# Kernel optimization log

Hardware: AMD Instinct MI355X
Metric: run time of the kernel (lower is better)

## Reference

```python
import jax, jax.numpy as jnp
import numpy as np

EMBED_DIM = 256
H = 80
W = 80
N_HEADS = 8
N_POINTS = 4
B = 8


def sine_pe(C, h, w):
    # LoFTR-style PositionEncodingSine, returns [1, C, h, w]
    y_pos = jnp.cumsum(jnp.ones((h, w), jnp.float32), axis=0)[None]
    x_pos = jnp.cumsum(jnp.ones((h, w), jnp.float32), axis=1)[None]
    div = jnp.exp(jnp.arange(0, C // 2, 2, dtype=jnp.float32) * (-np.log(10000.0) / (C // 2)))[:, None, None]
    pe = jnp.zeros((C, h, w), jnp.float32)
    pe = pe.at[0::4].set(jnp.sin(x_pos * div))
    pe = pe.at[1::4].set(jnp.cos(x_pos * div))
    pe = pe.at[2::4].set(jnp.sin(y_pos * div))
    pe = pe.at[3::4].set(jnp.cos(y_pos * div))
    return pe[None]


def make_reference_points(h, w):
    # Faithful to the original (W-major flatten, (col, row) stacking)
    gr = np.linspace(0, 1, w)
    gc = np.linspace(0, 1, h)
    R, Cg = np.meshgrid(gr, gc, indexing='ij')  # (w, h)
    ref = np.stack((Cg, R), -1).reshape(-1, 2)  # [w*h, 2]
    return jnp.asarray(ref, jnp.float32)


def setup_inputs():
    key = jax.random.key(0)
    ks = jax.random.split(key, 8)
    C = EMBED_DIM
    s = 1.0 / np.sqrt(C)
    return {
        'query': jax.random.normal(ks[0], (B, C, H, W), jnp.float32),
        'value': jax.random.normal(ks[1], (B, C, H, W), jnp.float32),
        'W_value': jax.random.normal(ks[2], (C, C), jnp.float32) * s,
        'b_value': jnp.zeros((C,), jnp.float32),
        'W_off': jax.random.normal(ks[3], (C, N_HEADS * N_POINTS * 2), jnp.float32) * 0.01,
        'b_off': jax.random.normal(ks[4], (N_HEADS * N_POINTS * 2,), jnp.float32) * 0.5,
        'W_attn': jax.random.normal(ks[5], (C, N_HEADS * N_POINTS), jnp.float32) * s,
        'b_attn': jnp.zeros((N_HEADS * N_POINTS,), jnp.float32),
        'W_out': jax.random.normal(ks[6], (C, C), jnp.float32) * s,
        'b_out': jnp.zeros((C,), jnp.float32),
    }


def _deform_attn_core(q, v, ref, W_off, b_off, W_attn, b_attn):
    # q: [B, Nq, C] queries; v: [B, H*W, C] projected values; ref: [Nq, 2]
    Bq, Nq, C = q.shape
    hd = C // N_HEADS
    off = (q @ W_off + b_off).reshape(Bq, Nq, N_HEADS, N_POINTS, 2)
    aw = jax.nn.softmax((q @ W_attn + b_attn).reshape(Bq, Nq, N_HEADS, N_POINTS), axis=-1)
    norm = jnp.array([W, H], jnp.float32)  # offset normalizer (W, H), num_levels=1
    loc = ref[None, :, None, None, :] + off / norm  # [B, Nq, Hn, P, 2], normalized (x, y)
    loc = loc.transpose(0, 2, 1, 3, 4)  # [B, Hn, Nq, P, 2]
    # grid_sample(align_corners=False, padding_mode='zeros'): pixel = loc*size - 0.5
    x = loc[..., 0] * W - 0.5
    y = loc[..., 1] * H - 0.5
    x0f = jnp.floor(x); y0f = jnp.floor(y)
    wx = x - x0f; wy = y - y0f
    x0 = x0f.astype(jnp.int32); y0 = y0f.astype(jnp.int32)
    vh = v.reshape(Bq, H * W, N_HEADS, hd).transpose(0, 2, 1, 3)  # [B, Hn, HW, hd]

    def gather(ix, iy):
        valid = (ix >= 0) & (ix < W) & (iy >= 0) & (iy < H)
        idx = jnp.clip(iy, 0, H - 1) * W + jnp.clip(ix, 0, W - 1)  # [B, Hn, Nq, P]
        g = jnp.take_along_axis(vh, idx.reshape(Bq, N_HEADS, -1, 1), axis=2)
        return g.reshape(Bq, N_HEADS, Nq, N_POINTS, hd) * valid[..., None].astype(v.dtype)

    samp = (gather(x0, y0) * ((1 - wx) * (1 - wy))[..., None]
            + gather(x0 + 1, y0) * (wx * (1 - wy))[..., None]
            + gather(x0, y0 + 1) * ((1 - wx) * wy)[..., None]
            + gather(x0 + 1, y0 + 1) * (wx * wy)[..., None])  # [B, Hn, Nq, P, hd]
    out = jnp.einsum('bhqpd,bhqp->bqhd', samp, aw.transpose(0, 2, 1, 3))
    return out.reshape(Bq, Nq, C)


def reference(query, value, W_value, b_value, W_off, b_off, W_attn, b_attn, W_out, b_out):
    pe = sine_pe(EMBED_DIM, H, W)
    q = query + pe
    qf = q.reshape(B, EMBED_DIM, H * W).transpose(0, 2, 1)      # [B, Nq, C]
    vf = value.reshape(B, EMBED_DIM, H * W).transpose(0, 2, 1)  # [B, Nv, C]
    vproj = vf @ W_value + b_value
    ref = make_reference_points(H, W)
    attn = _deform_attn_core(qf, vproj, ref, W_off, b_off, W_attn, b_attn)
    attn = attn @ W_out + b_out
    attn = attn + qf  # mmcv MSDeformAttn residual (dropout identity at eval)
    out_img = attn.transpose(0, 2, 1).reshape(B, EMBED_DIM, H, W)
    # nn.Upsample(size=(H, W), bilinear) on an (H, W) map is identity (need_downsample=False)
    return (out_img + value, out_img)
```

## Files before the change

### kernel.cpp

```cpp
#include <hip/hip_runtime.h>
#include <hip/hip_bf16.h>
#include <stdint.h>

#define HH 80
#define WW 80
#define NQ 6400
#define CD 256
#define BB 8
#define OUT_HALF 13107200
#define PE_NEG 0.0719557841560639f

typedef __attribute__((ext_vector_type(4))) float f32x4;
typedef __bf16 bf16_t;
typedef __attribute__((ext_vector_type(8))) __bf16 bf16x8;

using gp1_t = const __attribute__((address_space(1))) void*;
using lp3_t = __attribute__((address_space(3))) void*;

__device__ __forceinline__ void gload_lds16(const void* g, void* l) {
    __builtin_amdgcn_global_load_lds((gp1_t)g, (lp3_t)l, 16, 0, 0);
}

__global__ __launch_bounds__(256) void wprep_kernel(const float* __restrict__ Wv,
                                                    const float* __restrict__ Woff,
                                                    const float* __restrict__ Wattn,
                                                    const float* __restrict__ Wout,
                                                    bf16_t* __restrict__ WvT,
                                                    bf16_t* __restrict__ WoaT,
                                                    bf16_t* __restrict__ WoT) {
    int idx = blockIdx.x * 256 + threadIdx.x;
    if (idx < 65536) {
        int cp = idx >> 8, c = idx & 255;
        WvT[idx] = (bf16_t)Wv[c * 256 + cp];
        WoT[idx] = (bf16_t)Wout[c * 256 + cp];
    }
    if (idx < 96 * 256) {
        int j = idx >> 8, c = idx & 255;
        WoaT[idx] = (bf16_t)(j < 64 ? Woff[c * 64 + j] : Wattn[c * 32 + (j - 64)]);
    }
}

__global__ __launch_bounds__(256, 3) void gemm_vproj(const float* __restrict__ V,
                                                     const bf16_t* __restrict__ Y,
                                                     const float* __restrict__ bias,
                                                     bf16_t* __restrict__ D) {
    __shared__ __align__(16) bf16_t lx[128 * 72];
    __shared__ __align__(16) bf16_t ly[128 * 64];
    int b = blockIdx.x & 7;
    int nloc = (blockIdx.x >> 3) * 128;
    int m0 = b * NQ + nloc;
    int c0 = blockIdx.y * 128;
    const float* src = V + (size_t)b * CD * NQ + nloc;
    int tid = threadIdx.x, wv = tid >> 6, ln = tid & 63;
    f32x4 acc[4][4] = {};
    int wr = (wv >> 1) * 64, wc = (wv & 1) * 64;
    int nl = tid & 31;
    for (int kt = 0; kt < 4; ++kt) {
#pragma unroll
        for (int q8 = 0; q8 < 4; ++q8) {
            int q = wv * 4 + q8;
            int row = q * 8 + (ln >> 3);
            int jj = (ln & 7) ^ (row & 7);
            gload_lds16((const char*)Y + ((size_t)(c0 + row)) * 512 + (size_t)kt * 128 + jj * 16,
                        (char*)ly + q * 1024);
        }
#pragma unroll
        for (int i = 0; i < 4; ++i) {
            int kp = (tid >> 5) + i * 8;
            int k = kp * 2;
            const float* s0 = src + (size_t)(kt * 64 + k) * NQ;
#pragma unroll
            for (int l = 0; l < 4; ++l) {
                int n = nl + 32 * l;
                float v0 = s0[n];
                float v1 = s0[NQ + n];
                union { bf16_t h[2]; uint32_t u; } pk;
                pk.h[0] = (bf16_t)v0; pk.h[1] = (bf16_t)v1;
                *(uint32_t*)((char*)lx + n * 144 + k * 2) = pk.u;
            }
        }
        __syncthreads();
#pragma unroll
        for (int ks = 0; ks < 2; ++ks) {
            bf16x8 xa[4], yb[4];
#pragma unroll
            for (int i = 0; i < 4; i++) {
                int m = wr + i * 16 + (ln & 15);
                xa[i] = *(const bf16x8*)((const char*)lx + m * 144 + ks * 64 + (ln >> 4) * 16);
                int n = wc + i * 16 + (ln & 15);
                int cn = (ks * 4 + (ln >> 4)) ^ (n & 7);
                yb[i] = *(const bf16x8*)((const char*)ly + n * 128 + cn * 16);
            }
#pragma unroll
            for (int i = 0; i < 4; i++)
#pragma unroll
                for (int j = 0; j < 4; j++)
                    acc[i][j] = __builtin_amdgcn_mfma_f32_16x16x32_bf16(xa[i], yb[j], acc[i][j], 0, 0, 0);
        }
        __syncthreads();
    }
#pragma unroll
    for (int i = 0; i < 4; i++)
#pragma unroll
        for (int j = 0; j < 4; j++) {
            int col = c0 + wc + j * 16 + (ln & 15);
            float bv = bias[col];
#pragma unroll
            for (int rg = 0; rg < 4; rg++) {
                int row = m0 + wr + i * 16 + (ln >> 4) * 4 + rg;
                D[(size_t)row * 256 + col] = (bf16_t)(acc[i][j][rg] + bv);
            }
        }
}

__global__ __launch_bounds__(256, 2) void oa_sample_out(
        const float* __restrict__ Q,
        const bf16_t* __restrict__ Woa,
        const float* __restrict__ boff,
        const float* __restrict__ battn,
        const bf16_t* __restrict__ vp,
        const bf16_t* __restrict__ WoT,
        const float* __restrict__ bout,
        const float* __restrict__ value,
        float* __restrict__ out) {
    __shared__ __align__(16) char smem[67072];
    char* sampL = smem;
    bf16_t* lx = (bf16_t*)(smem + 32768);
    bf16_t* ly = (bf16_t*)(smem + 41984);
    bf16_t* wx = (bf16_t*)(smem + 32768);
    float* tile = (float*)(smem + 32768);
    bf16_t* oaT = (bf16_t*)(smem + 54272);

    int bid = blockIdx.x;
    int b = bid & 7;
    int nloc = (bid >> 3) * 64;
    int tid = threadIdx.x, wv = tid >> 6, ln = tid & 63;
    const float* src = Q + (size_t)b * CD * NQ + nloc;
    int nl = tid & 31;

    {
        f32x4 acc[1][6] = {};
        for (int kt = 0; kt < 4; ++kt) {
#pragma unroll
            for (int q3 = 0; q3 < 3; ++q3) {
                int q = wv * 3 + q3;
                int row = q * 8 + (ln >> 3);
                int jj = (ln & 7) ^ (row & 7);
                gload_lds16((const char*)Woa + ((size_t)row) * 512 + (size_t)kt * 128 + jj * 16,
                            (char*)ly + q * 1024);
            }
#pragma unroll
            for (int i = 0; i < 4; ++i) {
                int kp = (tid >> 5) + i * 8;
                int k = kp * 2;
                int c = kt * 64 + k;
                float d = __expf((float)(2 * (c >> 2)) * -PE_NEG);
                const float* s0 = src + (size_t)c * NQ;
#pragma unroll
                for (int l = 0; l < 2; ++l) {
                    int n = nl + 32 * l;
                    int p = nloc + n;
                    int h = p / WW, w = p - h * WW;
                    float pos = (c & 2) ? (float)(h + 1) : (float)(w + 1);
                    float sv, cv;
                    __sincosf(pos * d, &sv, &cv);
                    float v0 = s0[n] + sv;
                    float v1 = s0[NQ + n] + cv;
                    union { bf16_t hh[2]; uint32_t u; } pk;
                    pk.hh[0] = (bf16_t)v0; pk.hh[1] = (bf16_t)v1;
                    *(uint32_t*)((char*)lx + n * 144 + k * 2) = pk.u;
                }
            }
            __syncthreads();
#pragma unroll
            for (int ks = 0; ks < 2; ++ks) {
                bf16x8 xa, yb[6];
                int m = wv * 16 + (ln & 15);
                xa = *(const bf16x8*)((const char*)lx + m * 144 + ks * 64 + (ln >> 4) * 16);
#pragma unroll
                for (int j = 0; j < 6; j++) {
                    int n = j * 16 + (ln & 15);
                    int cn = (ks * 4 + (ln >> 4)) ^ (n & 7);
                    yb[j] = *(const bf16x8*)((const char*)ly + n * 128 + cn * 16);
                }
#pragma unroll
                for (int j = 0; j < 6; j++)
                    acc[0][j] = __builtin_amdgcn_mfma_f32_16x16x32_bf16(xa, yb[j], acc[0][j], 0, 0, 0);
            }
            __syncthreads();
        }
#pragma unroll
        for (int j = 0; j < 6; j++) {
            int col = j * 16 + (ln & 15);
            float bv = col < 64 ? boff[col] : battn[col - 64];
#pragma unroll
            for (int rg = 0; rg < 4; rg++) {
                int rloc = wv * 16 + (ln >> 4) * 4 + rg;
                oaT[rloc * 100 + col] = (bf16_t)(acc[0][j][rg] + bv);
            }
        }
    }
    __syncthreads();

    {
        int h = (tid >> 1) & 7, sh = tid & 1;
        const bf16_t* vb = vp + (size_t)b * NQ * CD + h * 32 + sh * 16;
#pragma unroll
        for (int rnd = 0; rnd < 4; ++rnd) {
            int q = rnd * 16 + (tid >> 4);
            int n = nloc + q;
            const bf16_t* sq = oaT + q * 100;
            float l0 = (float)sq[64 + h * 4 + 0], l1 = (float)sq[64 + h * 4 + 1];
            float l2 = (float)sq[64 + h * 4 + 2], l3 = (float)sq[64 + h * 4 + 3];
            float mx = fmaxf(fmaxf(l0, l1), fmaxf(l2, l3));
            float e0 = __expf(l0 - mx), e1 = __expf(l1 - mx), e2 = __expf(l2 - mx), e3 = __expf(l3 - mx);
            float inv = 1.f / (e0 + e1 + e2 + e3);
            float aw[4] = {e0 * inv, e1 * inv, e2 * inv, e3 * inv};
            float xb = (float)(n % WW) * (80.f / 79.f) - 0.5f;
            float yb = (float)(n / WW) * (80.f / 79.f) - 0.5f;
            float wgt[16];
            int idx[16];
#pragma unroll
            for (int p = 0; p < 4; p++) {
                float x = xb + (float)sq[h * 8 + p * 2];
                float y = yb + (float)sq[h * 8 + p * 2 + 1];
                float x0f = floorf(x), y0f = floorf(y);
                float wx_ = x - x0f, wy_ = y - y0f;
                int ix = (int)x0f, iy = (int)y0f;
                bool vx0 = (unsigned)ix < (unsigned)WW, vx1 = (unsigned)(ix + 1) < (unsigned)WW;
                bool vy0 = (unsigned)iy < (unsigned)HH, vy1 = (unsigned)(iy + 1) < (unsigned)HH;
                int cx0 = min(max(ix, 0), WW - 1), cx1 = min(max(ix + 1, 0), WW - 1);
                int cy0 = min(max(iy, 0), HH - 1), cy1 = min(max(iy + 1, 0), HH - 1);
                float ap = aw[p];
                wgt[p * 4 + 0] = (vx0 && vy0) ? ap * (1.f - wx_) * (1.f - wy_) : 0.f;
                wgt[p * 4 + 1] = (vx1 && vy0) ? ap * wx_ * (1.f - wy_) : 0.f;
                wgt[p * 4 + 2] = (vx0 && vy1) ? ap * (1.f - wx_) * wy_ : 0.f;
                wgt[p * 4 + 3] = (vx1 && vy1) ? ap * wx_ * wy_ : 0.f;
                idx[p * 4 + 0] = cy0 * WW + cx0;
                idx[p * 4 + 1] = cy0 * WW + cx1;
                idx[p * 4 + 2] = cy1 * WW + cx0;
                idx[p * 4 + 3] = cy1 * WW + cx1;
            }
            float fac[16];
#pragma unroll
            for (int j = 0; j < 16; j++) fac[j] = 0.f;
#pragma unroll
            for (int pc = 0; pc < 16; ++pc) {
                const bf16x8* p8 = (const bf16x8*)(vb + (size_t)idx[pc] * CD);
                bf16x8 v0 = p8[0], v1 = p8[1];
                float w = wgt[pc];
#pragma unroll
                for (int j = 0; j < 8; j++) fac[j] += (float)v0[j] * w;
#pragma unroll
                for (int j = 0; j < 8; j++) fac[8 + j] += (float)v1[j] * w;
            }
            bf16x8 o0, o1;
#pragma unroll
            for (int j = 0; j < 8; j++) { o0[j] = (bf16_t)fac[j]; o1[j] = (bf16_t)fac[8 + j]; }
            int c0 = 4 * h + 2 * sh;
            *(bf16x8*)(sampL + q * 512 + ((c0 ^ (q & 7)) * 16)) = o0;
            *(bf16x8*)(sampL + q * 512 + (((c0 + 1) ^ (q & 7)) * 16)) = o1;
        }
    }
    __syncthreads();

    const float* qp = Q + (size_t)b * CD * NQ;
    const float* vvp = value + (size_t)b * CD * NQ;
    float* o0p = out + (size_t)b * CD * NQ;
    float* o1p = out + OUT_HALF + (size_t)b * CD * NQ;
    for (int p = 0; p < 2; ++p) {
        int cb = p * 128;
        f32x4 acc[4][2] = {};
        for (int kt = 0; kt < 4; ++kt) {
#pragma unroll
            for (int q8 = 0; q8 < 4; ++q8) {
                int q = wv * 4 + q8;
                int row = q * 8 + (ln >> 3);
                int jj = (ln & 7) ^ (row & 7);
                gload_lds16((const char*)WoT + ((size_t)(cb + row)) * 512 + (size_t)kt * 128 + jj * 16,
                            (char*)wx + q * 1024);
            }
            __syncthreads();
#pragma unroll
            for (int ks = 0; ks < 2; ++ks) {
                bf16x8 xa[4], yb[2];
#pragma unroll
                for (int i = 0; i < 4; i++) {
                    int m = (wv >> 1) * 64 + i * 16 + (ln & 15);
                    int ch = (ks * 4 + (ln >> 4)) ^ (m & 7);
                    xa[i] = *(const bf16x8*)((const char*)wx + m * 128 + ch * 16);
                }
#pragma unroll
                for (int j = 0; j < 2; j++) {
                    int nr = (wv & 1) * 32 + j * 16 + (ln & 15);
                    int cj = kt * 8 + ks * 4 + (ln >> 4);
                    yb[j] = *(const bf16x8*)(sampL + nr * 512 + ((cj ^ (nr & 7)) * 16));
                }
#pragma unroll
                for (int i = 0; i < 4; i++)
#pragma unroll
                    for (int j = 0; j < 2; j++)
                        acc[i][j] = __builtin_amdgcn_mfma_f32_16x16x32_bf16(xa[i], yb[j], acc[i][j], 0, 0, 0);
            }
            __syncthreads();
        }
#pragma unroll
        for (int hp = 0; hp < 2; ++hp) {
            if ((wv >> 1) == hp) {
#pragma unroll
                for (int i = 0; i < 4; i++)
#pragma unroll
                    for (int j = 0; j < 2; j++) {
                        int c = (wv & 1) * 32 + j * 16 + (ln & 15);
#pragma unroll
                        for (int rg = 0; rg < 4; rg++) {
                            int r = i * 16 + (ln >> 4) * 4 + rg;
                            tile[r * 68 + c] = acc[i][j][rg] + bout[cb + hp * 64 + r];
                        }
                    }
            }
            __syncthreads();
            int g4 = (tid & 15) * 4;
            int rowbase = tid >> 4;
#pragma unroll
            for (int jj = 0; jj < 4; ++jj) {
                int r = rowbase + jj * 16;
                int crow = cb + hp * 64 + r;
                size_t off = (size_t)crow * NQ + nloc + g4;
                f32x4 tv = *(const f32x4*)&tile[r * 68 + g4];
                f32x4 qv = *(const f32x4*)(qp + off);
                f32x4 vv = *(const f32x4*)(vvp + off);
                float d = __expf((float)(2 * (crow >> 2)) * -PE_NEG);
                bool useY = (crow & 2) != 0, odd = (crow & 1) != 0;
                f32x4 pv;
#pragma unroll
                for (int e = 0; e < 4; ++e) {
                    int n = nloc + g4 + e;
                    int hh = n / WW, ww = n - hh * WW;
                    float pos = useY ? (float)(hh + 1) : (float)(ww + 1);
                    float sv, cv;
                    __sincosf(pos * d, &sv, &cv);
                    pv[e] = odd ? cv : sv;
                }
                f32x4 o1v = tv + qv + pv;
                *(f32x4*)(o1p + off) = o1v;
                *(f32x4*)(o0p + off) = o1v + vv;
            }
            __syncthreads();
        }
    }
}

extern "C" void kernel_launch(void* const* d_in, const int* in_sizes, int n_in,
                              void* d_out, int out_size, void* d_ws, size_t ws_size,
                              hipStream_t stream) {
    const float* query   = (const float*)d_in[0];
    const float* value   = (const float*)d_in[1];
    const float* W_value = (const float*)d_in[2];
    const float* b_value = (const float*)d_in[3];
    const float* W_off   = (const float*)d_in[4];
    const float* b_off   = (const float*)d_in[5];
    const float* W_attn  = (const float*)d_in[6];
    const float* b_attn  = (const float*)d_in[7];
    const float* W_out   = (const float*)d_in[8];
    const float* b_out   = (const float*)d_in[9];
    float* out = (float*)d_out;
    char* ws = (char*)d_ws;

    bf16_t* WvT   = (bf16_t*)(ws + 0);
    bf16_t* WoT   = (bf16_t*)(ws + 131072);
    bf16_t* WoaT  = (bf16_t*)(ws + 262144);
    bf16_t* vprojB= (bf16_t*)(ws + 311296);

    wprep_kernel<<<256, 256, 0, stream>>>(W_value, W_off, W_attn, W_out, WvT, WoaT, WoT);
    gemm_vproj<<<dim3(400, 2), 256, 0, stream>>>(value, WvT, b_value, vprojB);
    oa_sample_out<<<800, 256, 0, stream>>>(query, WoaT, b_off, b_attn, vprojB,
                                           WoT, b_out, value, out);
}
```

Before: 102.4 us.

## Run fused offset/sample/output kernel with 512 threads and smaller shared memory

The fused offset-projection, bilinear-sampling and output-projection kernel now uses 512 threads per block instead of 256, and every phase's work split is redone so each wave handles half as many rows or tiles. The oaT buffer is aliased onto the lx/ly staging region, cutting shared memory from about 67 KB to 54 KB so more blocks can be resident per CU. The aim is more waves in flight to hide the latency of the gather and global loads. The cost is fewer accumulators and less reuse per wave, and the 512-thread launch bound caps registers per thread.

```diff
diff --git a/kernel.cpp b/kernel.cpp
--- a/kernel.cpp
+++ b/kernel.cpp
@@ -113,7 +113,7 @@
         }
 }
 
-__global__ __launch_bounds__(256, 2) void oa_sample_out(
+__global__ __launch_bounds__(512, 4) void oa_sample_out(
         const float* __restrict__ Q,
         const bf16_t* __restrict__ Woa,
         const float* __restrict__ boff,
@@ -123,81 +123,83 @@
         const float* __restrict__ bout,
         const float* __restrict__ value,
         float* __restrict__ out) {
-    __shared__ __align__(16) char smem[67072];
+    __shared__ __align__(16) char smem[54272];
     char* sampL = smem;
     bf16_t* lx = (bf16_t*)(smem + 32768);
     bf16_t* ly = (bf16_t*)(smem + 41984);
+    bf16_t* oaT = (bf16_t*)(smem + 32768);
     bf16_t* wx = (bf16_t*)(smem + 32768);
     float* tile = (float*)(smem + 32768);
-    bf16_t* oaT = (bf16_t*)(smem + 54272);
 
     int bid = blockIdx.x;
     int b = bid & 7;
     int nloc = (bid >> 3) * 64;
     int tid = threadIdx.x, wv = tid >> 6, ln = tid & 63;
     const float* src = Q + (size_t)b * CD * NQ + nloc;
-    int nl = tid & 31;
-
-    {
-        f32x4 acc[1][6] = {};
-        for (int kt = 0; kt < 4; ++kt) {
-#pragma unroll
-            for (int q3 = 0; q3 < 3; ++q3) {
-                int q = wv * 3 + q3;
-                int row = q * 8 + (ln >> 3);
-                int jj = (ln & 7) ^ (row & 7);
-                gload_lds16((const char*)Woa + ((size_t)row) * 512 + (size_t)kt * 128 + jj * 16,
-                            (char*)ly + q * 1024);
-            }
+
+    f32x4 accA[3] = {};
+    for (int kt = 0; kt < 4; ++kt) {
+        {
+            int q = wv;
+            int row = q * 8 + (ln >> 3);
+            int jj = (ln & 7) ^ (row & 7);
+            gload_lds16((const char*)Woa + ((size_t)row) * 512 + (size_t)kt * 128 + jj * 16,
+                        (char*)ly + q * 1024);
+            if (wv < 4) {
+                int q2 = 8 + wv;
+                int row2 = q2 * 8 + (ln >> 3);
+                int jj2 = (ln & 7) ^ (row2 & 7);
+                gload_lds16((const char*)Woa + ((size_t)row2) * 512 + (size_t)kt * 128 + jj2 * 16,
+                            (char*)ly + q2 * 1024);
+            }
+        }
+        {
+            int n = tid & 63;
+            int p = nloc + n;
+            int hh = p / WW, ww = p - hh * WW;
 #pragma unroll
             for (int i = 0; i < 4; ++i) {
-                int kp = (tid >> 5) + i * 8;
+                int kp = (tid >> 6) + i * 8;
                 int k = kp * 2;
                 int c = kt * 64 + k;
                 float d = __expf((float)(2 * (c >> 2)) * -PE_NEG);
                 const float* s0 = src + (size_t)c * NQ;
-#pragma unroll
-                for (int l = 0; l < 2; ++l) {
-                    int n = nl + 32 * l;
-                    int p = nloc + n;
-                    int h = p / WW, w = p - h * WW;
-                    float pos = (c & 2) ? (float)(h + 1) : (float)(w + 1);
-                    float sv, cv;
-                    __sincosf(pos * d, &sv, &cv);
-                    float v0 = s0[n] + sv;
-                    float v1 = s0[NQ + n] + cv;
-                    union { bf16_t hh[2]; uint32_t u; } pk;
-                    pk.hh[0] = (bf16_t)v0; pk.hh[1] = (bf16_t)v1;
-                    *(uint32_t*)((char*)lx + n * 144 + k * 2) = pk.u;
-                }
-            }
-            __syncthreads();
-#pragma unroll
-            for (int ks = 0; ks < 2; ++ks) {
-                bf16x8 xa, yb[6];
-                int m = wv * 16 + (ln & 15);
-                xa = *(const bf16x8*)((const char*)lx + m * 144 + ks * 64 + (ln >> 4) * 16);
-#pragma unroll
-                for (int j = 0; j < 6; j++) {
-                    int n = j * 16 + (ln & 15);
-                    int cn = (ks * 4 + (ln >> 4)) ^ (n & 7);
-                    yb[j] = *(const bf16x8*)((const char*)ly + n * 128 + cn * 16);
-                }
-#pragma unroll
-                for (int j = 0; j < 6; j++)
-                    acc[0][j] = __builtin_amdgcn_mfma_f32_16x16x32_bf16(xa, yb[j], acc[0][j], 0, 0, 0);
-            }
-            __syncthreads();
-        }
-#pragma unroll
-        for (int j = 0; j < 6; j++) {
-            int col = j * 16 + (ln & 15);
-            float bv = col < 64 ? boff[col] : battn[col - 64];
-#pragma unroll
-            for (int rg = 0; rg < 4; rg++) {
-                int rloc = wv * 16 + (ln >> 4) * 4 + rg;
-                oaT[rloc * 100 + col] = (bf16_t)(acc[0][j][rg] + bv);
-            }
+                float pos = (c & 2) ? (float)(hh + 1) : (float)(ww + 1);
+                float sv, cv;
+                __sincosf(pos * d, &sv, &cv);
+                float v0 = s0[n] + sv;
+                float v1 = s0[NQ + n] + cv;
+                union { bf16_t h2[2]; uint32_t u; } pk;
+                pk.h2[0] = (bf16_t)v0; pk.h2[1] = (bf16_t)v1;
+                *(uint32_t*)((char*)lx + n * 144 + k * 2) = pk.u;
+            }
+        }
+        __syncthreads();
+#pragma unroll
+        for (int ks = 0; ks < 2; ++ks) {
+            bf16x8 xa, yb[3];
+            int m = (wv >> 1) * 16 + (ln & 15);
+            xa = *(const bf16x8*)((const char*)lx + m * 144 + ks * 64 + (ln >> 4) * 16);
+#pragma unroll
+            for (int j = 0; j < 3; j++) {
+                int n = ((wv & 1) * 3 + j) * 16 + (ln & 15);
+                int cn = (ks * 4 + (ln >> 4)) ^ (n & 7);
+                yb[j] = *(const bf16x8*)((const char*)ly + n * 128 + cn * 16);
+            }
+#pragma unroll
+            for (int j = 0; j < 3; j++)
+                accA[j] = __builtin_amdgcn_mfma_f32_16x16x32_bf16(xa, yb[j], accA[j], 0, 0, 0);
+        }
+        __syncthreads();
+    }
+#pragma unroll
+    for (int j = 0; j < 3; j++) {
+        int col = ((wv & 1) * 3 + j) * 16 + (ln & 15);
+        float bv = col < 64 ? boff[col] : battn[col - 64];
+#pragma unroll
+        for (int rg = 0; rg < 4; rg++) {
+            int rloc = (wv >> 1) * 16 + (ln >> 4) * 4 + rg;
+            oaT[rloc * 100 + col] = (bf16_t)(accA[j][rg] + bv);
         }
     }
     __syncthreads();
@@ -206,8 +208,8 @@
         int h = (tid >> 1) & 7, sh = tid & 1;
         const bf16_t* vb = vp + (size_t)b * NQ * CD + h * 32 + sh * 16;
 #pragma unroll
-        for (int rnd = 0; rnd < 4; ++rnd) {
-            int q = rnd * 16 + (tid >> 4);
+        for (int rnd = 0; rnd < 2; ++rnd) {
+            int q = rnd * 32 + (tid >> 4);
             int n = nloc + q;
             const bf16_t* sq = oaT + q * 100;
             float l0 = (float)sq[64 + h * 4 + 0], l1 = (float)sq[64 + h * 4 + 1];
@@ -268,13 +270,14 @@
     const float* vvp = value + (size_t)b * CD * NQ;
     float* o0p = out + (size_t)b * CD * NQ;
     float* o1p = out + OUT_HALF + (size_t)b * CD * NQ;
+    int mg = wv >> 1, nh = wv & 1;
     for (int p = 0; p < 2; ++p) {
         int cb = p * 128;
-        f32x4 acc[4][2] = {};
+        f32x4 acc[2][2] = {};
         for (int kt = 0; kt < 4; ++kt) {
 #pragma unroll
-            for (int q8 = 0; q8 < 4; ++q8) {
-                int q = wv * 4 + q8;
+            for (int q8 = 0; q8 < 2; ++q8) {
+                int q = wv * 2 + q8;
                 int row = q * 8 + (ln >> 3);
                 int jj = (ln & 7) ^ (row & 7);
                 gload_lds16((const char*)WoT + ((size_t)(cb + row)) * 512 + (size_t)kt * 128 + jj * 16,
@@ -283,21 +286,21 @@
             __syncthreads();
 #pragma unroll
             for (int ks = 0; ks < 2; ++ks) {
-                bf16x8 xa[4], yb[2];
-#pragma unroll
-                for (int i = 0; i < 4; i++) {
-                    int m = (wv >> 1) * 64 + i * 16 + (ln & 15);
+                bf16x8 xa[2], yb[2];
+#pragma unroll
+                for (int i = 0; i < 2; i++) {
+                    int m = mg * 32 + i * 16 + (ln & 15);
                     int ch = (ks * 4 + (ln >> 4)) ^ (m & 7);
                     xa[i] = *(const bf16x8*)((const char*)wx + m * 128 + ch * 16);
                 }
 #pragma unroll
                 for (int j = 0; j < 2; j++) {
-                    int nr = (wv & 1) * 32 + j * 16 + (ln & 15);
+                    int nr = nh * 32 + j * 16 + (ln & 15);
                     int cj = kt * 8 + ks * 4 + (ln >> 4);
                     yb[j] = *(const bf16x8*)(sampL + nr * 512 + ((cj ^ (nr & 7)) * 16));
                 }
 #pragma unroll
-                for (int i = 0; i < 4; i++)
+                for (int i = 0; i < 2; i++)
 #pragma unroll
                     for (int j = 0; j < 2; j++)
                         acc[i][j] = __builtin_amdgcn_mfma_f32_16x16x32_bf16(xa[i], yb[j], acc[i][j], 0, 0, 0);
@@ -306,15 +309,15 @@
         }
 #pragma unroll
         for (int hp = 0; hp < 2; ++hp) {
-            if ((wv >> 1) == hp) {
-#pragma unroll
-                for (int i = 0; i < 4; i++)
+            if ((wv >> 2) == hp) {
+#pragma unroll
+                for (int i = 0; i < 2; i++)
 #pragma unroll
                     for (int j = 0; j < 2; j++) {
-                        int c = (wv & 1) * 32 + j * 16 + (ln & 15);
+                        int c = nh * 32 + j * 16 + (ln & 15);
 #pragma unroll
                         for (int rg = 0; rg < 4; rg++) {
-                            int r = i * 16 + (ln >> 4) * 4 + rg;
+                            int r = (mg & 1) * 32 + i * 16 + (ln >> 4) * 4 + rg;
                             tile[r * 68 + c] = acc[i][j][rg] + bout[cb + hp * 64 + r];
                         }
                     }
@@ -323,8 +326,8 @@
             int g4 = (tid & 15) * 4;
             int rowbase = tid >> 4;
 #pragma unroll
-            for (int jj = 0; jj < 4; ++jj) {
-                int r = rowbase + jj * 16;
+            for (int jj = 0; jj < 2; ++jj) {
+                int r = rowbase + jj * 32;
                 int crow = cb + hp * 64 + r;
                 size_t off = (size_t)crow * NQ + nloc + g4;
                 f32x4 tv = *(const f32x4*)&tile[r * 68 + g4];
@@ -374,6 +377,6 @@
 
     wprep_kernel<<<256, 256, 0, stream>>>(W_value, W_off, W_attn, W_out, WvT, WoaT, WoT);
     gemm_vproj<<<dim3(400, 2), 256, 0, stream>>>(value, WvT, b_value, vprojB);
-    oa_sample_out<<<800, 256, 0, stream>>>(query, WoaT, b_off, b_attn, vprojB,
+    oa_sample_out<<<800, 512, 0, stream>>>(query, WoaT, b_off, b_attn, vprojB,
                                            WoT, b_out, value, out);
 }
```

New measurement: 109.7 us. 7.1% more time.
